# Kernel optimization log

Hardware: AMD Instinct MI355X
Metric: run time of the kernel (lower is better)

## Reference

```python
import jax, jax.numpy as jnp
import numpy as np

B, S, HID = 4, 4096, 1024
HEADS, D = 8, 128          # head_dim = HID // HEADS
NSEG, SEGLEN = 16, 256     # SEGLEN = S // NSEG
E, I = 16, 512             # num_experts, intermediate_size


def setup_inputs() -> dict:
    key = jax.random.key(0)
    ks = jax.random.split(key, 8)
    return {
        "x": jax.random.normal(ks[0], (B, S, HID), jnp.float32),
        "W_mh": jax.random.normal(ks[1], (HID, HID), jnp.float32) * (1.0 / np.sqrt(HID)),
        "b_mh": jax.random.normal(ks[2], (HID,), jnp.float32) * 0.02,
        "W_merge": jax.random.normal(ks[3], (HID, HID), jnp.float32) * (1.0 / np.sqrt(HID)),
        "b_merge": jnp.zeros((HID,), jnp.float32),
        "expert_embeddings": jax.random.normal(ks[4], (D, E), jnp.float32) * (1.0 / np.sqrt(D)),
        "first_linear": jax.random.normal(ks[5], (E, I, D), jnp.float32) * (1.0 / np.sqrt(D)),
        "second_linear": jax.random.normal(ks[6], (E, D, I), jnp.float32) * (1.0 / np.sqrt(I)),
    }


def reference(x, W_mh, b_mh, W_merge, b_merge, expert_embeddings, first_linear, second_linear):
    # multi-head projection
    x = x @ W_mh.T + b_mh                                   # [B,S,HID]
    # split into segments/heads (faithful to torch reshape order)
    x = x.reshape(B, NSEG, SEGLEN, HEADS, D)                # [B,N,L,H,D]
    avg = jnp.mean(x, axis=2)                               # [B,N,H,D]
    # router: softmax over experts
    ew = jax.nn.softmax(jnp.einsum('bnhd,de->bnhe', avg, expert_embeddings), axis=-1)
    # merge expert weight matrices (equivalent to torch's broadcast-mul-sum)
    m1 = jnp.einsum('eid,bnhe->bnhid', first_linear, ew)    # [B,N,H,I,D]
    m2 = jnp.einsum('edi,bnhe->bnhdi', second_linear, ew)   # [B,N,H,D,I]
    # NOTE: torch uses reshape (not permute) here -> mixes seglen/head axes; replicate.
    xr = x.reshape(B, NSEG, HEADS, SEGLEN, D)               # [B,N,H,L,D]
    # causal shift: segment s uses weights from segment s-1
    x_causal = xr[:, 1:]
    h = jax.nn.relu(jnp.einsum('bnhld,bnhid->bnhli', x_causal, m1[:, :-1]))
    res = jnp.einsum('bnhli,bnhdi->bnhld', h, m2[:, :-1])   # [B,N-1,H,L,D]
    # segment 0 special case (no_grad in torch -> stop_gradient)
    h0 = jax.nn.relu(jnp.einsum('bhld,bhid->bhli', xr[:, 0], m1[:, 0]))
    r0 = jnp.einsum('bhli,bhdi->bhld', h0, m2[:, 0])
    r0 = jax.lax.stop_gradient(r0)[:, None]                 # [B,1,H,L,D]
    out = jnp.concatenate([r0, res], axis=1)                # [B,N,H,L,D]
    out = out.reshape(B, S, HEADS, D).reshape(B, S, HID)
    return out @ W_merge.T + b_merge
```

## Files before the change

kernel.cpp:

```cpp
#include <hip/hip_runtime.h>
#include <hip/hip_bf16.h>

typedef _Float16 f16;
typedef f16 f16x2 __attribute__((ext_vector_type(2)));
typedef f16 f16x4 __attribute__((ext_vector_type(4)));
typedef f16 f16x8 __attribute__((ext_vector_type(8)));
typedef float f32x2 __attribute__((ext_vector_type(2)));
typedef float f32x4 __attribute__((ext_vector_type(4)));

#define MFMA16(a, b, c) __builtin_amdgcn_mfma_f32_16x16x32_f16(a, b, c, 0, 0, 0)

__device__ __forceinline__ void glds16(const void* g, void* l) {
    __builtin_amdgcn_global_load_lds(
        (const __attribute__((address_space(1))) unsigned int*)g,
        (__attribute__((address_space(3))) unsigned int*)l, 16, 0, 0);
}

#define VM8 asm volatile("s_waitcnt vmcnt(8)" ::: "memory")
#define VM6 asm volatile("s_waitcnt vmcnt(6)" ::: "memory")
#define VM4 asm volatile("s_waitcnt vmcnt(4)" ::: "memory")
#define VM0 asm volatile("s_waitcnt vmcnt(0)" ::: "memory")
#define VMN do {} while (0)
#define SB0 __builtin_amdgcn_sched_barrier(0)

__global__ __launch_bounds__(256) void cvt_kernel(const float* __restrict__ s,
                                                  f16* __restrict__ d, int n) {
    int i = (blockIdx.x * 256 + threadIdx.x) * 8;
    if (i >= n) return;
    float4 a = *(const float4*)(s + i);
    float4 b = *(const float4*)(s + i + 4);
    f16x8 h;
    h[0] = (f16)a.x; h[1] = (f16)a.y; h[2] = (f16)a.z; h[3] = (f16)a.w;
    h[4] = (f16)b.x; h[5] = (f16)b.y; h[6] = (f16)b.z; h[7] = (f16)b.w;
    *(f16x8*)(d + i) = h;
}

template <int MH, int NH, bool LOADA>
__device__ __forceinline__ void phase_rw(const f16* Aslab, const f16* Bslab,
                                         f16x8 (&af)[4][2], f16x8 (&bf)[2][2],
                                         int cl, int q, int wm, int wn) {
    if (LOADA) {
#pragma unroll
        for (int mt = 0; mt < 4; ++mt)
#pragma unroll
            for (int ks = 0; ks < 2; ++ks)
                af[mt][ks] =
                    *(const f16x8*)&Aslab[(wm * 64 + mt * 16 + cl) * 64 +
                                          ((ks * 4 + q) ^ (cl & 7)) * 8];
    }
#pragma unroll
    for (int nt = 0; nt < 2; ++nt)
#pragma unroll
        for (int ks = 0; ks < 2; ++ks)
            bf[nt][ks] = *(const f16x8*)&Bslab[(wn * 32 + nt * 16 + cl) * 64 +
                                               ((ks * 4 + q) ^ (cl & 7)) * 8];
}

template <int MH, int NH>
__device__ __forceinline__ void phase_mm(f16x8 (&af)[4][2], f16x8 (&bf)[2][2],
                                         f32x4 (&acc)[8][4]) {
    __builtin_amdgcn_s_setprio(1);
#pragma unroll
    for (int mt = 0; mt < 4; ++mt)
#pragma unroll
        for (int nt = 0; nt < 2; ++nt)
#pragma unroll
            for (int ks = 0; ks < 2; ++ks)
                acc[MH * 4 + mt][NH * 2 + nt] =
                    MFMA16(af[mt][ks], bf[nt][ks], acc[MH * 4 + mt][NH * 2 + nt]);
    __builtin_amdgcn_s_setprio(0);
}

__device__ __forceinline__ void stage_half(const f16* gsrc, int ldk, f16* ldst,
                                           int w, int lane) {
#pragma unroll
    for (int j = 0; j < 2; ++j) {
        int idx = j * 512 + w * 64 + lane;
        int rr = idx >> 3;
        int gs = (idx & 7) ^ (rr & 7);
        glds16(gsrc + (size_t)rr * ldk + gs * 8, ldst + (j * 512 + w * 64) * 8);
    }
}

#define SA(DB, H, KT) stage_half(A16 + (size_t)(mb * 256 + (H)*128) * K + (KT)*64, \
                                 K, Ad[DB][H], w, lane)
#define SBm(DB, H, KT) stage_half(Bw + (size_t)(nb * 256 + (H)*128) * K + (KT)*64, \
                                  K, Bd[DB][H], w, lane)

#define PH(DB, MH, NH, LA, STAGE, VMC)                                    \
    phase_rw<MH, NH, LA>(Ad[DB][MH], Bd[DB][NH], af, bf, cl, q, wm, wn);  \
    STAGE;                                                                \
    SB0; __builtin_amdgcn_s_barrier(); SB0;                               \
    phase_mm<MH, NH>(af, bf, acc);                                        \
    VMC;                                                                  \
    SB0; __builtin_amdgcn_s_barrier(); SB0;

template <bool OUT_F16, bool COLSUM>
__global__ __launch_bounds__(512, 2) void gemm256_kernel(
    const f16* __restrict__ A16, const f16* __restrict__ Bw,
    const float* __restrict__ bias, void* __restrict__ C_,
    float* __restrict__ colsum, int M, int N, int K) {
    __shared__ f16 Ad[2][2][128 * 64];
    __shared__ f16 Bd[2][2][128 * 64];
    const int tid = threadIdx.x;
    const int lane = tid & 63;
    const int w = tid >> 6;
    const int wm = w >> 2, wn = w & 3;
    const int q = lane >> 4, cl = lane & 15;
    const int nblk = N >> 8;
    const int cpx = (int)gridDim.x >> 3;
    const int logical = ((int)blockIdx.x & 7) * cpx + ((int)blockIdx.x >> 3);
    const int mb = logical / nblk, nb = logical % nblk;

    f32x4 acc[8][4] = {};
    f16x8 af[4][2], bf[2][2];
    const int ITERS = (K >> 6) / 2;

    SA(0, 0, 0); SBm(0, 0, 0); SBm(0, 1, 0); SA(0, 1, 0);
    SA(1, 0, 1); SBm(1, 0, 1);
    VM8;
    SB0; __builtin_amdgcn_s_barrier(); SB0;

#pragma unroll 1
    for (int i = 0; i < ITERS - 1; ++i) {
        const int k2 = 2 * i;
        PH(0, 0, 0, true,  SA(1, 1, k2 + 1),  VM8)
        PH(0, 0, 1, false, SBm(1, 1, k2 + 1), VM8)
        PH(0, 1, 0, true,  SA(0, 0, k2 + 2),  VMN)
        PH(0, 1, 1, false, SBm(0, 0, k2 + 2), VM8)
        PH(1, 0, 0, true,  SBm(0, 1, k2 + 2), VM6)
        PH(1, 0, 1, false, SA(0, 1, k2 + 2),  VMN)
        PH(1, 1, 0, true,  SA(1, 0, k2 + 3),  VMN)
        PH(1, 1, 1, false, SBm(1, 0, k2 + 3), VM8)
    }
    {
        const int kl = 2 * ITERS - 1;
        PH(0, 0, 0, true,  SA(1, 1, kl),  VM8)
        PH(0, 0, 1, false, SBm(1, 1, kl), VM8)
        PH(0, 1, 0, true,  VMN,           VMN)
        PH(0, 1, 1, false, VMN,           VM4)
        PH(1, 0, 0, true,  VMN,           VM0)
        PH(1, 0, 1, false, VMN,           VMN)
        PH(1, 1, 0, true,  VMN,           VMN)
        PH(1, 1, 1, false, VMN,           VMN)
    }

#pragma unroll
    for (int mt7 = 0; mt7 < 8; ++mt7) {
#pragma unroll
        for (int nt4 = 0; nt4 < 4; ++nt4) {
            int row0 = mb * 256 + (mt7 >> 2) * 128 + wm * 64 + (mt7 & 3) * 16 + q * 4;
            int col = nb * 256 + (nt4 >> 1) * 128 + wn * 32 + (nt4 & 1) * 16 + cl;
            float bv = bias[col];
#pragma unroll
            for (int r = 0; r < 4; ++r) {
                float v = acc[mt7][nt4][r] + bv;
                if (OUT_F16)
                    ((f16*)C_)[(size_t)(row0 + r) * N + col] = (f16)v;
                else
                    ((float*)C_)[(size_t)(row0 + r) * N + col] = v;
            }
        }
    }

    if (COLSUM) {
        float cs[4];
#pragma unroll
        for (int nt4 = 0; nt4 < 4; ++nt4) {
            int col = nb * 256 + (nt4 >> 1) * 128 + wn * 32 + (nt4 & 1) * 16 + cl;
            float s = 32.f * bias[col];
#pragma unroll
            for (int mt7 = 0; mt7 < 8; ++mt7)
#pragma unroll
                for (int r = 0; r < 4; ++r) s += acc[mt7][nt4][r];
            s += __shfl_xor(s, 16);
            s += __shfl_xor(s, 32);
            cs[nt4] = s;
        }
        float* S = (float*)Ad;
        __syncthreads();
        if (q == 0) {
#pragma unroll
            for (int nt4 = 0; nt4 < 4; ++nt4) S[w * 64 + nt4 * 16 + cl] = cs[nt4];
        }
        __syncthreads();
        if (tid < 256) {
            int col = tid;
            int quad = col >> 7, ciq = col & 127;
            int wn2 = ciq >> 5, sub = (ciq >> 4) & 1, cll = col & 15;
            int idx = wn2 * 64 + (quad * 2 + sub) * 16 + cll;
            colsum[(size_t)mb * N + nb * 256 + col] = S[idx] + S[256 + idx];
        }
    }
}

__global__ __launch_bounds__(64) void router_kernel(const float* __restrict__ colsum,
                                                    const float* __restrict__ emb,
                                                    float* __restrict__ ew) {
    const int t = blockIdx.x;
    const int bn = t >> 3, h = t & 7;
    const int lane = threadIdx.x;
    float acc = 0.f;
    const float* p = colsum + (size_t)bn * 1024 + h * 128;
    if (lane < 16) {
        const float sc = 1.f / 256.f;
        for (int d = 0; d < 128; ++d)
            acc = fmaf(p[d] * sc, emb[d * 16 + lane], acc);
    }
    float m = acc;
#pragma unroll
    for (int o = 8; o; o >>= 1) m = fmaxf(m, __shfl_xor(m, o));
    float pr = __expf(acc - m);
    float s = pr;
#pragma unroll
    for (int o = 8; o; o >>= 1) s += __shfl_xor(s, o);
    if (lane < 16) ew[t * 16 + lane] = pr / s;
}

__global__ __launch_bounds__(256) void mix_kernel(const float* __restrict__ ew,
                                                  const float* __restrict__ FL,
                                                  const float* __restrict__ SL,
                                                  f16* __restrict__ m1h,
                                                  f16* __restrict__ m2h) {
    const int bid = blockIdx.x;
    const int which = bid >> 10;
    const int tg = (bid >> 6) & 15;
    const int chunk = bid & 63;
    const float* src = which ? SL : FL;
    f16* dst = which ? m2h : m1h;
    const int tid = threadIdx.x;
    const int e0 = chunk * 1024 + tid * 4;

    f32x4 fl[16];
#pragma unroll
    for (int e = 0; e < 16; ++e)
        fl[e] = *(const f32x4*)(src + (size_t)e * 65536 + e0);

    const float* wbase = ew + (size_t)tg * 32 * 16;
    float wc[16];
#pragma unroll
    for (int e = 0; e < 16; ++e) wc[e] = wbase[e];

#pragma unroll 1
    for (int tt = 0; tt < 32; ++tt) {
        float wn2[16];
        if (tt < 31) {
#pragma unroll
            for (int e = 0; e < 16; ++e) wn2[e] = wbase[(tt + 1) * 16 + e];
        }
        f32x4 a = {0.f, 0.f, 0.f, 0.f};
#pragma unroll
        for (int e = 0; e < 16; ++e) {
            a[0] = fmaf(wc[e], fl[e][0], a[0]);
            a[1] = fmaf(wc[e], fl[e][1], a[1]);
            a[2] = fmaf(wc[e], fl[e][2], a[2]);
            a[3] = fmaf(wc[e], fl[e][3], a[3]);
        }
        f16x4 h;
        h[0] = (f16)a[0]; h[1] = (f16)a[1]; h[2] = (f16)a[2]; h[3] = (f16)a[3];
        *(f16x4*)(dst + (size_t)(tg * 32 + tt) * 65536 + e0) = h;
        if (tt < 31) {
#pragma unroll
            for (int e = 0; e < 16; ++e) wc[e] = wn2[e];
        }
    }
}

__device__ __forceinline__ void stage_m1c(const f16* m1c, f16* dst, int tid) {
#pragma unroll
    for (int j = 0; j < 4; ++j) {
        int idx = j * 256 + tid;
        int row = idx >> 4, g = idx & 15;
        glds16(m1c + (size_t)row * 128 + (g ^ (row & 7)) * 8, dst + (idx & ~63) * 8);
    }
}
__device__ __forceinline__ void stage_m2c(const f16* m2c, f16* dst, int tid) {
#pragma unroll
    for (int j = 0; j < 4; ++j) {
        int idx = j * 256 + tid;
        int row = idx >> 3, g = idx & 7;
        glds16(m2c + (size_t)row * 512 + (g ^ (row & 7)) * 8, dst + (idx & ~63) * 8);
    }
}

__global__ __launch_bounds__(256) void mlp_kernel(const f16* __restrict__ Xg,
                                                  const f16* __restrict__ m1h,
                                                  const f16* __restrict__ m2h,
                                                  f16* __restrict__ Yg) {
    __shared__ f16 Ws[128 * 64];
    __shared__ f16 Hs[128 * 64];
    const int cpx = (int)gridDim.x >> 3;
    const int logical = ((int)blockIdx.x & 7) * cpx + ((int)blockIdx.x >> 3);
    const int t = logical >> 1, lh = logical & 1;
    const int n = (t >> 3) & 15;
    const int tm = (n > 0) ? (t - 8) : t;
    const int tid = threadIdx.x;
    const int lane = tid & 63, w = tid >> 6;
    const int q = lane >> 4, cl = lane & 15;
    const int l0 = w * 32;

    const f16* Xsrc = Xg + (size_t)t * 32768 + lh * 16384;
    const f16* m1b = m1h + (size_t)tm * 65536;
    const f16* m2b = m2h + (size_t)tm * 65536;

    stage_m1c(m1b, Ws, tid);
    f16x8 xf[2][4];
#pragma unroll
    for (int lt = 0; lt < 2; ++lt) {
        int l = l0 + lt * 16 + cl;
#pragma unroll
        for (int ks = 0; ks < 4; ++ks)
            xf[lt][ks] = *(const f16x8*)(Xsrc + (size_t)l * 128 + ks * 32 + q * 8);
    }
    __syncthreads();

    f32x4 acc2[2][8] = {};
#pragma unroll 1
    for (int ic = 0; ic < 8; ++ic) {
#pragma unroll
        for (int it = 0; it < 4; ++it) {
            f16x8 af2[4];
#pragma unroll
            for (int ks = 0; ks < 4; ++ks) {
                int r = it * 16 + cl;
                af2[ks] = *(const f16x8*)&Ws[r * 128 +
                                             (((ks * 4 + q) ^ (r & 7))) * 8];
            }
            f32x4 a1[2] = {};
#pragma unroll
            for (int ks = 0; ks < 4; ++ks)
#pragma unroll
                for (int lt = 0; lt < 2; ++lt)
                    a1[lt] = MFMA16(af2[ks], xf[lt][ks], a1[lt]);
            int gi = 2 * it + (q >> 1);
            int sub = (q & 1) * 8;
#pragma unroll
            for (int lt = 0; lt < 2; ++lt) {
                int l = l0 + lt * 16 + cl;
                f16x4 hv;
                hv[0] = (f16)fmaxf(a1[lt][0], 0.f);
                hv[1] = (f16)fmaxf(a1[lt][1], 0.f);
                hv[2] = (f16)fmaxf(a1[lt][2], 0.f);
                hv[3] = (f16)fmaxf(a1[lt][3], 0.f);
                *(f16x4*)((char*)Hs + (size_t)l * 128 + ((gi ^ (l & 7)) << 4) + sub) =
                    hv;
            }
        }
        __syncthreads();
        stage_m2c(m2b + ic * 64, Ws, tid);
        __syncthreads();

        f16x8 hf[2][2];
#pragma unroll
        for (int lt = 0; lt < 2; ++lt)
#pragma unroll
            for (int ks = 0; ks < 2; ++ks) {
                int l = l0 + lt * 16 + cl;
                hf[lt][ks] =
                    *(const f16x8*)&Hs[l * 64 + (((ks * 4 + q) ^ (l & 7))) * 8];
            }
#pragma unroll
        for (int nt = 0; nt < 8; ++nt) {
            f16x8 bf2[2];
#pragma unroll
            for (int ks = 0; ks < 2; ++ks) {
                int d = nt * 16 + cl;
                bf2[ks] = *(const f16x8*)&Ws[d * 64 +
                                             (((ks * 4 + q) ^ (d & 7))) * 8];
            }
#pragma unroll
            for (int lt = 0; lt < 2; ++lt)
#pragma unroll
                for (int ks = 0; ks < 2; ++ks)
                    acc2[lt][nt] = MFMA16(hf[lt][ks], bf2[ks], acc2[lt][nt]);
        }
        __syncthreads();
        if (ic < 7) {
            stage_m1c(m1b + (size_t)(ic + 1) * 8192, Ws, tid);
            __syncthreads();
        }
    }

    f16* Yb = Yg + (size_t)t * 32768 + lh * 16384;
#pragma unroll
    for (int lt = 0; lt < 2; ++lt) {
#pragma unroll
        for (int nt = 0; nt < 8; ++nt) {
            int lr = l0 + lt * 16 + q * 4;
            int d = nt * 16 + cl;
#pragma unroll
            for (int r = 0; r < 4; ++r)
                Yb[(size_t)(lr + r) * 128 + d] = (f16)acc2[lt][nt][r];
        }
    }
}

extern "C" void kernel_launch(void* const* d_in, const int* in_sizes, int n_in,
                              void* d_out, int out_size, void* d_ws, size_t ws_size,
                              hipStream_t stream) {
    const float* x    = (const float*)d_in[0];
    const float* W_mh = (const float*)d_in[1];
    const float* b_mh = (const float*)d_in[2];
    const float* W_mg = (const float*)d_in[3];
    const float* b_mg = (const float*)d_in[4];
    const float* emb  = (const float*)d_in[5];
    const float* FL   = (const float*)d_in[6];
    const float* SL   = (const float*)d_in[7];

    char* ws = (char*)d_ws;
    f16*   X1h  = (f16*)(ws + 0);
    f16*   m1h  = (f16*)(ws + 33554432);
    f16*   X0h  = (f16*)(ws + 33554432);
    f16*   m2h  = (f16*)(ws + 100663296);
    f16*   Wmhh = (f16*)(ws + 167772160);
    f16*   Wmgh = (f16*)(ws + 169869312);
    float* csum = (float*)(ws + 171966464);
    float* ew   = (float*)(ws + 172228608);

    cvt_kernel<<<512, 256, 0, stream>>>(W_mh, Wmhh, 1048576);
    cvt_kernel<<<512, 256, 0, stream>>>(W_mg, Wmgh, 1048576);
    cvt_kernel<<<8192, 256, 0, stream>>>(x, X0h, 16777216);
    gemm256_kernel<true, true><<<256, 512, 0, stream>>>(X0h, Wmhh, b_mh, X1h,
                                                        csum, 16384, 1024, 1024);
    router_kernel<<<512, 64, 0, stream>>>(csum, emb, ew);
    mix_kernel<<<2048, 256, 0, stream>>>(ew, FL, SL, m1h, m2h);
    mlp_kernel<<<1024, 256, 0, stream>>>(X1h, m1h, m2h, X1h);
    gemm256_kernel<false, false><<<256, 512, 0, stream>>>(X1h, Wmgh, b_mg, d_out,
                                                          nullptr, 16384, 1024, 1024);
}
```

Baseline: 201.2 us.

## Shrink GEMM tiles to 128x128 with 256-thread blocks and reuse B fragments

Both projection GEMMs move from 256x256 tiles on 512-thread blocks to 128x128 tiles on 256-thread blocks, launching 1024 blocks instead of 256 so the grid fills the GPU's compute units more evenly. B fragments are now kept per N-half in registers and reloaded only on the phases that need them. Because each M tile now covers half a segment, the column-sum output holds two partial sums per segment, and the router adds them before averaging. Smaller tiles lower per-block arithmetic intensity and increase global traffic per FLOP.

```diff
diff --git a/kernel.cpp b/kernel.cpp
--- a/kernel.cpp
+++ b/kernel.cpp
@@ -35,85 +35,88 @@
     *(f16x8*)(d + i) = h;
 }
 
-template <int MH, int NH, bool LOADA>
+template <int MH, int NH, bool LOADA, bool LOADB>
 __device__ __forceinline__ void phase_rw(const f16* Aslab, const f16* Bslab,
-                                         f16x8 (&af)[4][2], f16x8 (&bf)[2][2],
+                                         f16x8 (&af)[2][2], f16x8 (&bfp)[2][2][2],
                                          int cl, int q, int wm, int wn) {
     if (LOADA) {
 #pragma unroll
-        for (int mt = 0; mt < 4; ++mt)
+        for (int mt = 0; mt < 2; ++mt)
 #pragma unroll
             for (int ks = 0; ks < 2; ++ks)
                 af[mt][ks] =
-                    *(const f16x8*)&Aslab[(wm * 64 + mt * 16 + cl) * 64 +
+                    *(const f16x8*)&Aslab[(wm * 32 + mt * 16 + cl) * 64 +
                                           ((ks * 4 + q) ^ (cl & 7)) * 8];
     }
-#pragma unroll
-    for (int nt = 0; nt < 2; ++nt)
-#pragma unroll
-        for (int ks = 0; ks < 2; ++ks)
-            bf[nt][ks] = *(const f16x8*)&Bslab[(wn * 32 + nt * 16 + cl) * 64 +
-                                               ((ks * 4 + q) ^ (cl & 7)) * 8];
+    if (LOADB) {
+#pragma unroll
+        for (int nt = 0; nt < 2; ++nt)
+#pragma unroll
+            for (int ks = 0; ks < 2; ++ks)
+                bfp[NH][nt][ks] =
+                    *(const f16x8*)&Bslab[(wn * 32 + nt * 16 + cl) * 64 +
+                                          ((ks * 4 + q) ^ (cl & 7)) * 8];
+    }
 }
 
 template <int MH, int NH>
-__device__ __forceinline__ void phase_mm(f16x8 (&af)[4][2], f16x8 (&bf)[2][2],
-                                         f32x4 (&acc)[8][4]) {
+__device__ __forceinline__ void phase_mm(f16x8 (&af)[2][2], f16x8 (&bfp)[2][2][2],
+                                         f32x4 (&acc)[4][4]) {
     __builtin_amdgcn_s_setprio(1);
 #pragma unroll
-    for (int mt = 0; mt < 4; ++mt)
+    for (int mt = 0; mt < 2; ++mt)
 #pragma unroll
         for (int nt = 0; nt < 2; ++nt)
 #pragma unroll
             for (int ks = 0; ks < 2; ++ks)
-                acc[MH * 4 + mt][NH * 2 + nt] =
-                    MFMA16(af[mt][ks], bf[nt][ks], acc[MH * 4 + mt][NH * 2 + nt]);
+                acc[MH * 2 + mt][NH * 2 + nt] =
+                    MFMA16(af[mt][ks], bfp[NH][nt][ks], acc[MH * 2 + mt][NH * 2 + nt]);
     __builtin_amdgcn_s_setprio(0);
 }
 
-__device__ __forceinline__ void stage_half(const f16* gsrc, int ldk, f16* ldst,
-                                           int w, int lane) {
+__device__ __forceinline__ void stage_slab(const f16* gsrc, int ldk, f16* ldst,
+                                           int tid) {
 #pragma unroll
     for (int j = 0; j < 2; ++j) {
-        int idx = j * 512 + w * 64 + lane;
+        int idx = j * 256 + tid;
         int rr = idx >> 3;
         int gs = (idx & 7) ^ (rr & 7);
-        glds16(gsrc + (size_t)rr * ldk + gs * 8, ldst + (j * 512 + w * 64) * 8);
-    }
-}
-
-#define SA(DB, H, KT) stage_half(A16 + (size_t)(mb * 256 + (H)*128) * K + (KT)*64, \
-                                 K, Ad[DB][H], w, lane)
-#define SBm(DB, H, KT) stage_half(Bw + (size_t)(nb * 256 + (H)*128) * K + (KT)*64, \
-                                  K, Bd[DB][H], w, lane)
-
-#define PH(DB, MH, NH, LA, STAGE, VMC)                                    \
-    phase_rw<MH, NH, LA>(Ad[DB][MH], Bd[DB][NH], af, bf, cl, q, wm, wn);  \
-    STAGE;                                                                \
-    SB0; __builtin_amdgcn_s_barrier(); SB0;                               \
-    phase_mm<MH, NH>(af, bf, acc);                                        \
-    VMC;                                                                  \
+        glds16(gsrc + (size_t)rr * ldk + gs * 8, ldst + (idx & ~63) * 8);
+    }
+}
+
+#define SA(DB, H, KT) stage_slab(A16 + (size_t)(mb * 128 + (H)*64) * K + (KT)*64, \
+                                 K, Ad[DB][H], tid)
+#define SBm(DB, H, KT) stage_slab(Bw + (size_t)(nb * 128 + (H)*64) * K + (KT)*64, \
+                                  K, Bd[DB][H], tid)
+
+#define PH(DB, MH_, NH_, LA, LB, STAGE, VMC)                                   \
+    phase_rw<MH_, NH_, LA, LB>(Ad[DB][MH_], Bd[DB][NH_], af, bfp, cl, q, wm, wn); \
+    STAGE;                                                                     \
+    SB0; __builtin_amdgcn_s_barrier(); SB0;                                    \
+    phase_mm<MH_, NH_>(af, bfp, acc);                                          \
+    VMC;                                                                       \
     SB0; __builtin_amdgcn_s_barrier(); SB0;
 
 template <bool OUT_F16, bool COLSUM>
-__global__ __launch_bounds__(512, 2) void gemm256_kernel(
+__global__ __launch_bounds__(256, 2) void gemm_kernel(
     const f16* __restrict__ A16, const f16* __restrict__ Bw,
     const float* __restrict__ bias, void* __restrict__ C_,
     float* __restrict__ colsum, int M, int N, int K) {
-    __shared__ f16 Ad[2][2][128 * 64];
-    __shared__ f16 Bd[2][2][128 * 64];
+    __shared__ f16 Ad[2][2][64 * 64];
+    __shared__ f16 Bd[2][2][64 * 64];
     const int tid = threadIdx.x;
     const int lane = tid & 63;
     const int w = tid >> 6;
-    const int wm = w >> 2, wn = w & 3;
+    const int wm = w >> 1, wn = w & 1;
     const int q = lane >> 4, cl = lane & 15;
-    const int nblk = N >> 8;
+    const int nblk = N >> 7;
     const int cpx = (int)gridDim.x >> 3;
     const int logical = ((int)blockIdx.x & 7) * cpx + ((int)blockIdx.x >> 3);
     const int mb = logical / nblk, nb = logical % nblk;
 
-    f32x4 acc[8][4] = {};
-    f16x8 af[4][2], bf[2][2];
+    f32x4 acc[4][4] = {};
+    f16x8 af[2][2], bfp[2][2][2];
     const int ITERS = (K >> 6) / 2;
 
     SA(0, 0, 0); SBm(0, 0, 0); SBm(0, 1, 0); SA(0, 1, 0);
@@ -124,33 +127,33 @@
 #pragma unroll 1
     for (int i = 0; i < ITERS - 1; ++i) {
         const int k2 = 2 * i;
-        PH(0, 0, 0, true,  SA(1, 1, k2 + 1),  VM8)
-        PH(0, 0, 1, false, SBm(1, 1, k2 + 1), VM8)
-        PH(0, 1, 0, true,  SA(0, 0, k2 + 2),  VMN)
-        PH(0, 1, 1, false, SBm(0, 0, k2 + 2), VM8)
-        PH(1, 0, 0, true,  SBm(0, 1, k2 + 2), VM6)
-        PH(1, 0, 1, false, SA(0, 1, k2 + 2),  VMN)
-        PH(1, 1, 0, true,  SA(1, 0, k2 + 3),  VMN)
-        PH(1, 1, 1, false, SBm(1, 0, k2 + 3), VM8)
+        PH(0, 0, 0, true,  true,  SA(1, 1, k2 + 1),  VM8)
+        PH(0, 0, 1, false, true,  SBm(1, 1, k2 + 1), VM8)
+        PH(0, 1, 0, true,  false, SA(0, 0, k2 + 2),  VMN)
+        PH(0, 1, 1, false, false, SBm(0, 0, k2 + 2), VM8)
+        PH(1, 0, 0, true,  true,  SBm(0, 1, k2 + 2), VM6)
+        PH(1, 0, 1, false, true,  SA(0, 1, k2 + 2),  VMN)
+        PH(1, 1, 0, true,  false, SA(1, 0, k2 + 3),  VMN)
+        PH(1, 1, 1, false, false, SBm(1, 0, k2 + 3), VM8)
     }
     {
         const int kl = 2 * ITERS - 1;
-        PH(0, 0, 0, true,  SA(1, 1, kl),  VM8)
-        PH(0, 0, 1, false, SBm(1, 1, kl), VM8)
-        PH(0, 1, 0, true,  VMN,           VMN)
-        PH(0, 1, 1, false, VMN,           VM4)
-        PH(1, 0, 0, true,  VMN,           VM0)
-        PH(1, 0, 1, false, VMN,           VMN)
-        PH(1, 1, 0, true,  VMN,           VMN)
-        PH(1, 1, 1, false, VMN,           VMN)
-    }
-
-#pragma unroll
-    for (int mt7 = 0; mt7 < 8; ++mt7) {
+        PH(0, 0, 0, true,  true,  SA(1, 1, kl),  VM8)
+        PH(0, 0, 1, false, true,  SBm(1, 1, kl), VM8)
+        PH(0, 1, 0, true,  false, VMN,           VMN)
+        PH(0, 1, 1, false, false, VMN,           VM4)
+        PH(1, 0, 0, true,  true,  VMN,           VM0)
+        PH(1, 0, 1, false, true,  VMN,           VMN)
+        PH(1, 1, 0, true,  false, VMN,           VMN)
+        PH(1, 1, 1, false, false, VMN,           VMN)
+    }
+
+#pragma unroll
+    for (int mt7 = 0; mt7 < 4; ++mt7) {
 #pragma unroll
         for (int nt4 = 0; nt4 < 4; ++nt4) {
-            int row0 = mb * 256 + (mt7 >> 2) * 128 + wm * 64 + (mt7 & 3) * 16 + q * 4;
-            int col = nb * 256 + (nt4 >> 1) * 128 + wn * 32 + (nt4 & 1) * 16 + cl;
+            int row0 = mb * 128 + (mt7 >> 1) * 64 + wm * 32 + (mt7 & 1) * 16 + q * 4;
+            int col = nb * 128 + (nt4 >> 1) * 64 + wn * 32 + (nt4 & 1) * 16 + cl;
             float bv = bias[col];
 #pragma unroll
             for (int r = 0; r < 4; ++r) {
@@ -167,10 +170,9 @@
         float cs[4];
 #pragma unroll
         for (int nt4 = 0; nt4 < 4; ++nt4) {
-            int col = nb * 256 + (nt4 >> 1) * 128 + wn * 32 + (nt4 & 1) * 16 + cl;
-            float s = 32.f * bias[col];
-#pragma unroll
-            for (int mt7 = 0; mt7 < 8; ++mt7)
+            float s = 0.f;
+#pragma unroll
+            for (int mt7 = 0; mt7 < 4; ++mt7)
 #pragma unroll
                 for (int r = 0; r < 4; ++r) s += acc[mt7][nt4][r];
             s += __shfl_xor(s, 16);
@@ -184,12 +186,13 @@
             for (int nt4 = 0; nt4 < 4; ++nt4) S[w * 64 + nt4 * 16 + cl] = cs[nt4];
         }
         __syncthreads();
-        if (tid < 256) {
-            int col = tid;
-            int quad = col >> 7, ciq = col & 127;
-            int wn2 = ciq >> 5, sub = (ciq >> 4) & 1, cll = col & 15;
-            int idx = wn2 * 64 + (quad * 2 + sub) * 16 + cll;
-            colsum[(size_t)mb * N + nb * 256 + col] = S[idx] + S[256 + idx];
+        if (tid < 128) {
+            int c = tid;
+            int NHq = c >> 6, wn2 = (c >> 5) & 1, sub = (c >> 4) & 1, cll = c & 15;
+            int idx = (NHq * 2 + sub) * 16 + cll;
+            int col = nb * 128 + c;
+            colsum[(size_t)mb * N + col] =
+                S[wn2 * 64 + idx] + S[(2 + wn2) * 64 + idx] + 128.f * bias[col];
         }
     }
 }
@@ -201,11 +204,11 @@
     const int bn = t >> 3, h = t & 7;
     const int lane = threadIdx.x;
     float acc = 0.f;
-    const float* p = colsum + (size_t)bn * 1024 + h * 128;
+    const float* p = colsum + (size_t)bn * 2048 + h * 128;
     if (lane < 16) {
         const float sc = 1.f / 256.f;
         for (int d = 0; d < 128; ++d)
-            acc = fmaf(p[d] * sc, emb[d * 16 + lane], acc);
+            acc = fmaf((p[d] + p[d + 1024]) * sc, emb[d * 16 + lane], acc);
     }
     float m = acc;
 #pragma unroll
@@ -415,16 +418,16 @@
     f16*   Wmhh = (f16*)(ws + 167772160);
     f16*   Wmgh = (f16*)(ws + 169869312);
     float* csum = (float*)(ws + 171966464);
-    float* ew   = (float*)(ws + 172228608);
+    float* ew   = (float*)(ws + 172490752);
 
     cvt_kernel<<<512, 256, 0, stream>>>(W_mh, Wmhh, 1048576);
     cvt_kernel<<<512, 256, 0, stream>>>(W_mg, Wmgh, 1048576);
     cvt_kernel<<<8192, 256, 0, stream>>>(x, X0h, 16777216);
-    gemm256_kernel<true, true><<<256, 512, 0, stream>>>(X0h, Wmhh, b_mh, X1h,
-                                                        csum, 16384, 1024, 1024);
+    gemm_kernel<true, true><<<1024, 256, 0, stream>>>(X0h, Wmhh, b_mh, X1h,
+                                                      csum, 16384, 1024, 1024);
     router_kernel<<<512, 64, 0, stream>>>(csum, emb, ew);
     mix_kernel<<<2048, 256, 0, stream>>>(ew, FL, SL, m1h, m2h);
     mlp_kernel<<<1024, 256, 0, stream>>>(X1h, m1h, m2h, X1h);
-    gemm256_kernel<false, false><<<256, 512, 0, stream>>>(X1h, Wmgh, b_mg, d_out,
-                                                          nullptr, 16384, 1024, 1024);
-}
+    gemm_kernel<false, false><<<1024, 256, 0, stream>>>(X1h, Wmgh, b_mg, d_out,
+                                                        nullptr, 16384, 1024, 1024);
+}
```

Result: no change. 204.9 us (+1.8%).
